# Kernel optimization log

Hardware: AMD Instinct MI355X
Metric: run time of the kernel (lower is better)

The kernel has to match this reference:

```python
import jax, jax.numpy as jnp
import numpy as np

N = 100000   # nodes
E = 600000   # edges
NF = 4       # node feat dim (3 pos + 1 scalar)
EF = 5       # edge feat dim
H = 128      # hidden dim


def setup_inputs() -> dict:
    key = jax.random.key(0)
    ks = jax.random.split(key, 9)

    def lin(k, fan_in, fan_out):
        return (jax.random.normal(k, (fan_in, fan_out), dtype=jnp.float32)
                * (1.0 / np.sqrt(fan_in)))

    x = jax.random.normal(ks[0], (N, NF), dtype=jnp.float32)
    edge_index = jax.random.randint(ks[1], (2, E), 0, N, dtype=jnp.int32)
    edge_attr = jax.random.normal(ks[2], (E, EF), dtype=jnp.float32)

    return {
        "x": x,
        "edge_attr": edge_attr,
        "W1": lin(ks[3], NF, H), "b1": jnp.zeros((H,), jnp.float32),
        "W2": lin(ks[4], H, H),  "b2": jnp.zeros((H,), jnp.float32),
        "Wm1": lin(ks[5], 2 * H + EF, H), "bm1": jnp.zeros((H,), jnp.float32),
        "Wm2": lin(ks[6], H, H),          "bm2": jnp.zeros((H,), jnp.float32),
        "Wm3": lin(ks[7], H, 1),          "bm3": jnp.zeros((1,), jnp.float32),
        "edge_index": edge_index,
    }


def reference(x, edge_attr, W1, b1, W2, b2, Wm1, bm1, Wm2, bm2, Wm3, bm3,
              edge_index):
    src, dst = edge_index[0], edge_index[1]
    n = x.shape[0]

    # GCNConv: add self-loops, symmetric D^{-1/2} A D^{-1/2} normalization.
    loop = jnp.arange(n, dtype=src.dtype)
    src_sl = jnp.concatenate([src, loop])
    dst_sl = jnp.concatenate([dst, loop])
    deg = jax.ops.segment_sum(jnp.ones_like(src_sl, dtype=x.dtype),
                              dst_sl, num_segments=n)
    dinv = jnp.where(deg > 0, jax.lax.rsqrt(deg), 0.0)
    enorm = dinv[src_sl] * dinv[dst_sl]          # [E + N]

    def gcn(h, W, b):
        h = h @ W                                 # transform then propagate
        msg = h[src_sl] * enorm[:, None]          # gather + scale
        return jax.ops.segment_sum(msg, dst_sl, num_segments=n) + b

    h = jax.nn.relu(gcn(x, W1, b1))
    h = gcn(h, W2, b2)

    # Edge classifier: gather endpoints, concat with edge features, MLP.
    edge_emb = jnp.concatenate([h[src], h[dst], edge_attr], axis=1)  # [E, 2H+EF]
    z = jax.nn.relu(edge_emb @ Wm1 + bm1)
    z = jax.nn.relu(z @ Wm2 + bm2)
    out = (z @ Wm3 + bm3)[:, 0]
    return jax.nn.sigmoid(out)
```

## Files before the change

kernel.cpp:

```cpp
#include <hip/hip_runtime.h>
#include <math.h>

#define TPB 256
#define SCAN_T 256
#define SCAN_I 4
#define SCAN_CHUNK 1024

typedef __attribute__((ext_vector_type(8))) short bf16x8;
typedef __attribute__((ext_vector_type(16))) float f32x16;

static __device__ __forceinline__ short f2bf(float a) {
  unsigned ua = __builtin_bit_cast(unsigned, a);
  ua = (ua + 0x7fffu + ((ua >> 16) & 1u)) >> 16;
  return (short)ua;
}
static __device__ __forceinline__ unsigned f2bf_pack(float a, float b) {
  unsigned ua = __builtin_bit_cast(unsigned, a);
  unsigned ub = __builtin_bit_cast(unsigned, b);
  ua = (ua + 0x7fffu + ((ua >> 16) & 1u)) >> 16;
  ub = (ub + 0x7fffu + ((ub >> 16) & 1u)) >> 16;
  return ua | (ub << 16);
}
static __device__ __forceinline__ float bflo(unsigned u) {
  return __builtin_bit_cast(float, u << 16);
}
static __device__ __forceinline__ float bfhi(unsigned u) {
  return __builtin_bit_cast(float, u & 0xffff0000u);
}

__global__ void k_zero_int(int* __restrict__ p, int n) {
  int t = blockIdx.x * TPB + threadIdx.x;
  if (t < n) p[t] = 0;
}

__global__ void k_hist(const int* __restrict__ dst, int* __restrict__ deg, int E) {
  int t = blockIdx.x * TPB + threadIdx.x;
  if (t < E) atomicAdd(&deg[dst[t]], 1);
}

__global__ __launch_bounds__(SCAN_T) void k_scan_local(const int* __restrict__ deg,
                                                       int* __restrict__ loc,
                                                       int* __restrict__ bsum,
                                                       float* __restrict__ dinv,
                                                       const float4* __restrict__ x4,
                                                       float4* __restrict__ xs, int N) {
  __shared__ int s[SCAN_T];
  int b = blockIdx.x, t = threadIdx.x;
  int base = b * SCAN_CHUNK + t * SCAN_I;
  int v[SCAN_I];
  int sum = 0;
#pragma unroll
  for (int u = 0; u < SCAN_I; u++) {
    int x = (base + u < N) ? deg[base + u] : 0;
    if (base + u < N) {
      float dv = rsqrtf((float)x + 1.0f);
      dinv[base + u] = dv;
      float4 xv = x4[base + u];
      xs[base + u] = make_float4(xv.x * dv, xv.y * dv, xv.z * dv, xv.w * dv);
    }
    v[u] = sum;
    sum += x;
  }
  s[t] = sum;
  __syncthreads();
#pragma unroll
  for (int off = 1; off < SCAN_T; off <<= 1) {
    int x = (t >= off) ? s[t - off] : 0;
    __syncthreads();
    s[t] += x;
    __syncthreads();
  }
  int excl = (t == 0) ? 0 : s[t - 1];
#pragma unroll
  for (int u = 0; u < SCAN_I; u++)
    if (base + u < N) loc[base + u] = v[u] + excl;
  if (t == SCAN_T - 1) bsum[b] = s[t];
}

__global__ void k_scan_block(int* __restrict__ bsum, int nb) {
  int t = threadIdx.x;
  int i0 = 2 * t, i1 = 2 * t + 1;
  int a = (i0 < nb) ? bsum[i0] : 0;
  int b = (i1 < nb) ? bsum[i1] : 0;
  int s = a + b;
#pragma unroll
  for (int off = 1; off < 64; off <<= 1) {
    int u = __shfl_up(s, off, 64);
    if (t >= off) s += u;
  }
  int excl = s - (a + b);
  if (i0 < nb) bsum[i0] = excl;
  if (i1 < nb) bsum[i1] = excl + a;
}

__global__ void k_scan_add(int* __restrict__ rowoff, const int* __restrict__ bsum,
                           int* __restrict__ cursor, int N) {
  int t = blockIdx.x * TPB + threadIdx.x;
  if (t >= N) return;
  int ro = rowoff[t] + bsum[t / SCAN_CHUNK];
  rowoff[t] = ro;
  cursor[t] = ro;
}

__global__ void k_fill_slots(const int* __restrict__ src, const int* __restrict__ dst,
                             int* __restrict__ cursor, int* __restrict__ slots,
                             int2* __restrict__ epair, int E) {
  int e = blockIdx.x * TPB + threadIdx.x;
  if (e >= E) return;
  int d = dst[e];
  int pos = atomicAdd(&cursor[d], 1);
  slots[pos] = src[e];
  epair[pos] = make_int2(e, d);
}

__global__ __launch_bounds__(256) void k_agg1(const float4* __restrict__ xs,
                                              const int* __restrict__ rowoff,
                                              const int* __restrict__ deg,
                                              const int* __restrict__ slots,
                                              const float* __restrict__ dinv,
                                              const float* __restrict__ W1,
                                              const float* __restrict__ b1,
                                              unsigned* __restrict__ h1, int N) {
  int u = threadIdx.x & 15;
  float w[4][8];
  float bb[8];
#pragma unroll
  for (int k = 0; k < 4; k++)
#pragma unroll
    for (int c = 0; c < 8; c++) w[k][c] = W1[k * 128 + u * 8 + c];
#pragma unroll
  for (int c = 0; c < 8; c++) bb[c] = b1[u * 8 + c];

  int g0 = (blockIdx.x * TPB + threadIdx.x) >> 4;
  int gstride = (gridDim.x * TPB) >> 4;
  for (int n = g0; n < N; n += gstride) {
    int start = rowoff[n], d = deg[n];
    float4 acc = make_float4(0.f, 0.f, 0.f, 0.f);
    for (int j = u; j < d; j += 16) {
      float4 v = xs[slots[start + j]];
      acc.x += v.x;
      acc.y += v.y;
      acc.z += v.z;
      acc.w += v.w;
    }
#pragma unroll
    for (int off = 8; off >= 1; off >>= 1) {
      acc.x += __shfl_xor(acc.x, off, 16);
      acc.y += __shfl_xor(acc.y, off, 16);
      acc.z += __shfl_xor(acc.z, off, 16);
      acc.w += __shfl_xor(acc.w, off, 16);
    }
    float4 xv = xs[n];
    acc.x += xv.x;
    acc.y += xv.y;
    acc.z += xv.z;
    acc.w += xv.w;
    float sc = dinv[n];
    uint4 o;
    unsigned* op = (unsigned*)&o;
#pragma unroll
    for (int c2 = 0; c2 < 4; c2++) {
      int c0 = 2 * c2, c1 = 2 * c2 + 1;
      float r0 = fmaf(acc.x, w[0][c0],
                      fmaf(acc.y, w[1][c0], fmaf(acc.z, w[2][c0], acc.w * w[3][c0])));
      float r1 = fmaf(acc.x, w[0][c1],
                      fmaf(acc.y, w[1][c1], fmaf(acc.z, w[2][c1], acc.w * w[3][c1])));
      r0 = fmaxf(fmaf(r0, sc, bb[c0]), 0.f);
      r1 = fmaxf(fmaf(r1, sc, bb[c1]), 0.f);
      op[c2] = f2bf_pack(r0, r1);
    }
    *(uint4*)&h1[(size_t)n * 64 + u * 4] = o;
  }
}

template <bool RELU>
__global__ void k_agg(const unsigned* __restrict__ ts, const int* __restrict__ rowoff,
                      const int* __restrict__ deg, const int* __restrict__ slots,
                      const float* __restrict__ dinv, const float* __restrict__ bias,
                      unsigned* __restrict__ hout, int N) {
  int t = blockIdx.x * TPB + threadIdx.x;
  int n = t >> 4;
  if (n >= N) return;
  int q = (t & 15) << 2;
  uint4 sv = *(const uint4*)&ts[(size_t)n * 64 + q];
  float a0 = bflo(sv.x), a1 = bfhi(sv.x), a2 = bflo(sv.y), a3 = bfhi(sv.y);
  float a4 = bflo(sv.z), a5 = bfhi(sv.z), a6 = bflo(sv.w), a7 = bfhi(sv.w);
  int start = rowoff[n], d = deg[n];
  for (int j0 = 0; j0 < d; j0 += 8) {
    int sl[8];
#pragma unroll
    for (int u = 0; u < 8; u++) {
      int jj = j0 + u;
      sl[u] = (jj < d) ? slots[start + jj] : -1;
    }
    uint4 v[8];
#pragma unroll
    for (int u = 0; u < 8; u++)
      v[u] = (sl[u] >= 0) ? *(const uint4*)&ts[(size_t)sl[u] * 64 + q]
                          : make_uint4(0u, 0u, 0u, 0u);
#pragma unroll
    for (int u = 0; u < 8; u++) {
      a0 += bflo(v[u].x);
      a1 += bfhi(v[u].x);
      a2 += bflo(v[u].y);
      a3 += bfhi(v[u].y);
      a4 += bflo(v[u].z);
      a5 += bfhi(v[u].z);
      a6 += bflo(v[u].w);
      a7 += bfhi(v[u].w);
    }
  }
  float sc = dinv[n];
  int col = q << 1;
  float4 b0 = *(const float4*)&bias[col];
  float4 b1 = *(const float4*)&bias[col + 4];
  a0 = a0 * sc + b0.x;
  a1 = a1 * sc + b0.y;
  a2 = a2 * sc + b0.z;
  a3 = a3 * sc + b0.w;
  a4 = a4 * sc + b1.x;
  a5 = a5 * sc + b1.y;
  a6 = a6 * sc + b1.z;
  a7 = a7 * sc + b1.w;
  if (RELU) {
    a0 = fmaxf(a0, 0.f);
    a1 = fmaxf(a1, 0.f);
    a2 = fmaxf(a2, 0.f);
    a3 = fmaxf(a3, 0.f);
    a4 = fmaxf(a4, 0.f);
    a5 = fmaxf(a5, 0.f);
    a6 = fmaxf(a6, 0.f);
    a7 = fmaxf(a7, 0.f);
  }
  uint4 p;
  p.x = f2bf_pack(a0, a1);
  p.y = f2bf_pack(a2, a3);
  p.z = f2bf_pack(a4, a5);
  p.w = f2bf_pack(a6, a7);
  *(uint4*)&hout[(size_t)n * 64 + q] = p;
}

template <bool BIAS, bool DINV>
__global__ __launch_bounds__(256, 2) void k_gemm_bf(const unsigned* __restrict__ A,
                                                    const float* __restrict__ W,
                                                    const float* __restrict__ bias,
                                                    const float* __restrict__ dinv,
                                                    unsigned* __restrict__ out, int N) {
  __shared__ unsigned sA[64 * 64];
  __shared__ float sDinv[64];
  int tid = threadIdx.x;
  int wv = tid >> 6, lane = tid & 63;
  int rg = wv >> 1, ch = wv & 1;
  int l31 = lane & 31, h = lane >> 5;

  bf16x8 wf[2][8];
  float bcol[2];
#pragma unroll
  for (int t = 0; t < 2; t++) {
    int col = ch * 64 + 2 * l31 + t;
#pragma unroll
    for (int kk = 0; kk < 8; kk++) {
      int kb = kk * 16 + h * 8;
      bf16x8 v;
#pragma unroll
      for (int u = 0; u < 8; u++) v[u] = f2bf(W[(kb + u) * 128 + col]);
      wf[t][kk] = v;
    }
    bcol[t] = BIAS ? bias[col] : 0.f;
  }

  int ntiles = (N + 63) >> 6;
  for (int tile = blockIdx.x; tile < ntiles; tile += gridDim.x) {
    __syncthreads();
    int row0 = tile << 6;
    for (int idx = tid; idx < 1024; idx += 256) {
      int r = idx >> 4, c4 = idx & 15;
      int n = row0 + r;
      uint4 v = (n < N) ? ((const uint4*)A)[(size_t)n * 16 + c4] : make_uint4(0, 0, 0, 0);
      *(uint4*)&sA[r * 64 + ((c4 * 4) ^ ((r & 15) << 2))] = v;
    }
    if (DINV && tid < 64) sDinv[tid] = (row0 + tid < N) ? dinv[row0 + tid] : 0.f;
    __syncthreads();

    int arow = rg * 32 + l31;
    const char* abase = (const char*)sA + arow * 256;
    int swz = (arow & 15) << 4;
    f32x16 acc[2];
#pragma unroll
    for (int t = 0; t < 2; t++) {
#pragma unroll
      for (int r = 0; r < 16; r++) acc[t][r] = 0.f;
    }
#pragma unroll
    for (int kk = 0; kk < 8; kk++) {
      bf16x8 a = *(const bf16x8*)(abase + ((kk * 32 + h * 16) ^ swz));
      acc[0] = __builtin_amdgcn_mfma_f32_32x32x16_bf16(a, wf[0][kk], acc[0], 0, 0, 0);
      acc[1] = __builtin_amdgcn_mfma_f32_32x32x16_bf16(a, wf[1][kk], acc[1], 0, 0, 0);
    }
#pragma unroll
    for (int r = 0; r < 16; r++) {
      int drow = (r & 3) + 8 * (r >> 2) + 4 * h;
      int n = row0 + rg * 32 + drow;
      if (n < N) {
        float v0 = acc[0][r] + bcol[0];
        float v1 = acc[1][r] + bcol[1];
        if (DINV) {
          float s = sDinv[rg * 32 + drow];
          v0 *= s;
          v1 *= s;
        }
        out[(size_t)n * 64 + ch * 32 + l31] = f2bf_pack(v0, v1);
      }
    }
  }
}

__global__ __launch_bounds__(512, 2) void k_gemm_dual(const unsigned* __restrict__ A,
                                                      const float* __restrict__ Wm1,
                                                      const float* __restrict__ bm1,
                                                      unsigned* __restrict__ out_s,
                                                      unsigned* __restrict__ out_d, int N) {
  __shared__ unsigned sA[64 * 64];
  int tid = threadIdx.x;
  int wv = tid >> 6, lane = tid & 63;
  int part = wv >> 2;
  int w4 = wv & 3;
  int rg = w4 >> 1, ch = w4 & 1;
  int l31 = lane & 31, h = lane >> 5;
  const float* W = Wm1 + (size_t)part * 128 * 128;
  unsigned* outp = part ? out_d : out_s;

  bf16x8 wf[2][8];
  float bcol[2];
#pragma unroll
  for (int t = 0; t < 2; t++) {
    int col = ch * 64 + 2 * l31 + t;
#pragma unroll
    for (int kk = 0; kk < 8; kk++) {
      int kb = kk * 16 + h * 8;
      bf16x8 v;
#pragma unroll
      for (int u = 0; u < 8; u++) v[u] = f2bf(W[(kb + u) * 128 + col]);
      wf[t][kk] = v;
    }
    bcol[t] = part ? 0.f : bm1[col];
  }

  int ntiles = (N + 63) >> 6;
  for (int tile = blockIdx.x; tile < ntiles; tile += gridDim.x) {
    __syncthreads();
    int row0 = tile << 6;
    for (int idx = tid; idx < 1024; idx += 512) {
      int r = idx >> 4, c4 = idx & 15;
      int n = row0 + r;
      uint4 v = (n < N) ? ((const uint4*)A)[(size_t)n * 16 + c4] : make_uint4(0, 0, 0, 0);
      *(uint4*)&sA[r * 64 + ((c4 * 4) ^ ((r & 15) << 2))] = v;
    }
    __syncthreads();

    int arow = rg * 32 + l31;
    const char* abase = (const char*)sA + arow * 256;
    int swz = (arow & 15) << 4;
    f32x16 acc[2];
#pragma unroll
    for (int t = 0; t < 2; t++) {
#pragma unroll
      for (int r = 0; r < 16; r++) acc[t][r] = 0.f;
    }
#pragma unroll
    for (int kk = 0; kk < 8; kk++) {
      bf16x8 a = *(const bf16x8*)(abase + ((kk * 32 + h * 16) ^ swz));
      acc[0] = __builtin_amdgcn_mfma_f32_32x32x16_bf16(a, wf[0][kk], acc[0], 0, 0, 0);
      acc[1] = __builtin_amdgcn_mfma_f32_32x32x16_bf16(a, wf[1][kk], acc[1], 0, 0, 0);
    }
#pragma unroll
    for (int r = 0; r < 16; r++) {
      int drow = (r & 3) + 8 * (r >> 2) + 4 * h;
      int n = row0 + rg * 32 + drow;
      if (n < N) {
        float v0 = acc[0][r] + bcol[0];
        float v1 = acc[1][r] + bcol[1];
        outp[(size_t)n * 64 + ch * 32 + l31] = f2bf_pack(v0, v1);
      }
    }
  }
}

__global__ __launch_bounds__(256, 3) void k_edge_mlp(
    const unsigned* __restrict__ a_s, const unsigned* __restrict__ a_d,
    const float* __restrict__ eattr, const int* __restrict__ slots,
    const int2* __restrict__ epair, const float* __restrict__ We,
    const float* __restrict__ Wm2, const float* __restrict__ bm2,
    const float* __restrict__ Wm3, const float* __restrict__ bm3,
    float* __restrict__ out, int E) {
  __shared__ unsigned sZ1[64 * 64];
  __shared__ float sEa[64][5];
  __shared__ int sSrc[64], sDst[64], sEid[64];
  __shared__ float sP[64][2];

  int tid = threadIdx.x;
  int wv = tid >> 6;
  int lane = tid & 63;
  int rg = wv >> 1;
  int ch = wv & 1;
  int l31 = lane & 31;
  int h = lane >> 5;

  bf16x8 bfr[2][8];
#pragma unroll
  for (int t = 0; t < 2; t++) {
    int col = ch * 64 + t * 32 + l31;
#pragma unroll
    for (int kk = 0; kk < 8; kk++) {
      int kb = kk * 16 + h * 8;
      bf16x8 v;
#pragma unroll
      for (int u = 0; u < 8; u++) v[u] = f2bf(Wm2[(kb + u) * 128 + col]);
      bfr[t][kk] = v;
    }
  }
  float wm3c[2], bm2c[2];
#pragma unroll
  for (int t = 0; t < 2; t++) {
    int col = ch * 64 + t * 32 + l31;
    wm3c[t] = Wm3[col];
    bm2c[t] = bm2[col];
  }
  float bm3v = bm3[0];
  float2 we[5];
#pragma unroll
  for (int j = 0; j < 5; j++) we[j] = *(const float2*)(We + j * 128 + 2 * lane);

  int ntiles = (E + 63) >> 6;
  for (int tile = blockIdx.x; tile < ntiles; tile += gridDim.x) {
    __syncthreads();
    int p0 = tile << 6;
    if (tid < 64) {
      int p = p0 + tid;
      int2 ed = (p < E) ? epair[p] : make_int2(0, 0);
      sSrc[tid] = (p < E) ? slots[p] : 0;
      sDst[tid] = ed.y;
      sEid[tid] = ed.x;
    }
    for (int idx = tid; idx < 320; idx += 256) {
      int r = idx / 5, j = idx - r * 5;
      int p = p0 + r;
      int e = (p < E) ? epair[p].x : 0;
      sEa[r][j] = (p < E) ? eattr[(size_t)e * 5 + j] : 0.f;
    }
    __syncthreads();

    unsigned ua[16], ud[16];
#pragma unroll
    for (int i = 0; i < 16; i++) {
      int r = wv * 16 + i;
      ua[i] = a_s[(size_t)sSrc[r] * 64 + lane];
      ud[i] = a_d[(size_t)sDst[r] * 64 + lane];
    }
#pragma unroll
    for (int i = 0; i < 16; i++) {
      int r = wv * 16 + i;
      float v0 = bflo(ua[i]) + bflo(ud[i]);
      float v1 = bfhi(ua[i]) + bfhi(ud[i]);
#pragma unroll
      for (int j = 0; j < 5; j++) {
        float ea = sEa[r][j];
        v0 = fmaf(ea, we[j].x, v0);
        v1 = fmaf(ea, we[j].y, v1);
      }
      v0 = fmaxf(v0, 0.f);
      v1 = fmaxf(v1, 0.f);
      sZ1[r * 64 + (lane ^ ((r & 15) << 2))] = f2bf_pack(v0, v1);
    }
    __syncthreads();

    int arow = rg * 32 + l31;
    const char* abase = (const char*)sZ1 + arow * 256;
    int swz = (arow & 15) << 4;
    float p16[16];
#pragma unroll
    for (int r = 0; r < 16; r++) p16[r] = 0.f;
#pragma unroll
    for (int t = 0; t < 2; t++) {
      f32x16 acc;
#pragma unroll
      for (int r = 0; r < 16; r++) acc[r] = 0.f;
#pragma unroll
      for (int kk = 0; kk < 8; kk++) {
        bf16x8 a = *(const bf16x8*)(abase + ((kk * 32 + h * 16) ^ swz));
        acc = __builtin_amdgcn_mfma_f32_32x32x16_bf16(a, bfr[t][kk], acc, 0, 0, 0);
      }
#pragma unroll
      for (int r = 0; r < 16; r++) {
        float z2 = fmaxf(acc[r] + bm2c[t], 0.f);
        p16[r] = fmaf(z2, wm3c[t], p16[r]);
      }
    }
#pragma unroll
    for (int r = 0; r < 16; r++) {
      float p = p16[r];
#pragma unroll
      for (int off = 16; off >= 1; off >>= 1) p += __shfl_xor(p, off, 32);
      if (l31 == 0) {
        int row = (r & 3) + 8 * (r >> 2) + 4 * h;
        sP[rg * 32 + row][ch] = p;
      }
    }
    __syncthreads();
    if (tid < 64) {
      int p = p0 + tid;
      if (p < E) {
        float pv = sP[tid][0] + sP[tid][1] + bm3v;
        out[sEid[tid]] = 1.f / (1.f + __expf(-pv));
      }
    }
  }
}

extern "C" void kernel_launch(void* const* d_in, const int* in_sizes, int n_in,
                              void* d_out, int out_size, void* d_ws, size_t ws_size,
                              hipStream_t stream) {
  const float* x = (const float*)d_in[0];
  const float* eattr = (const float*)d_in[1];
  const float* W1 = (const float*)d_in[2];
  const float* b1 = (const float*)d_in[3];
  const float* W2 = (const float*)d_in[4];
  const float* b2 = (const float*)d_in[5];
  const float* Wm1 = (const float*)d_in[6];
  const float* bm1 = (const float*)d_in[7];
  const float* Wm2 = (const float*)d_in[8];
  const float* bm2 = (const float*)d_in[9];
  const float* Wm3 = (const float*)d_in[10];
  const float* bm3 = (const float*)d_in[11];
  const int* ei = (const int*)d_in[12];
  int N = in_sizes[0] / 4;
  int E = in_sizes[12] / 2;
  const int* src = ei;
  const int* dst = ei + E;
  float* out = (float*)d_out;

  size_t npad = (size_t)((N + 63) & ~63);
  float* dinv = (float*)d_ws;
  float4* xs = (float4*)(dinv + npad);
  unsigned* U1 = (unsigned*)(xs + npad);
  unsigned* U2 = U1 + (size_t)N * 64;
  unsigned* U3 = U2 + (size_t)N * 64;
  unsigned* U4 = U3 + (size_t)N * 64;
  int* degi = (int*)(U4 + (size_t)N * 64);
  int* rowoff = degi + npad;
  int* cursor = rowoff + npad;
  int* bsum = cursor + npad;
  int* slots = bsum + 256;
  int2* epair = (int2*)(slots + ((E + 1) & ~1));

  int gN = (N + TPB - 1) / TPB;
  int gE = (E + TPB - 1) / TPB;
  int gN16 = (N * 16 + TPB - 1) / TPB;
  int nb1 = (N + SCAN_CHUNK - 1) / SCAN_CHUNK;

  k_zero_int<<<gN, TPB, 0, stream>>>(degi, N);
  k_hist<<<gE, TPB, 0, stream>>>(dst, degi, E);
  k_scan_local<<<nb1, SCAN_T, 0, stream>>>(degi, rowoff, bsum, dinv, (const float4*)x, xs, N);
  k_scan_block<<<1, 64, 0, stream>>>(bsum, nb1);
  k_scan_add<<<gN, TPB, 0, stream>>>(rowoff, bsum, cursor, N);
  k_fill_slots<<<gE, TPB, 0, stream>>>(src, dst, cursor, slots, epair, E);

  k_agg1<<<2048, TPB, 0, stream>>>(xs, rowoff, degi, slots, dinv, W1, b1, U2, N);

  k_gemm_bf<false, true><<<512, TPB, 0, stream>>>(U2, W2, nullptr, dinv, U1, N);
  k_agg<false><<<gN16, TPB, 0, stream>>>(U1, rowoff, degi, slots, dinv, b2, U3, N);

  k_gemm_dual<<<512, 512, 0, stream>>>(U3, Wm1, bm1, U2, U4, N);
  k_edge_mlp<<<2048, TPB, 0, stream>>>(U2, U4, eattr, slots, epair,
                                       Wm1 + 256 * 128, Wm2, bm2, Wm3, bm3, out, E);
}
```

Baseline: 281.6 us.

## Double-buffer edge metadata and prefetch next tile's source rows during MFMA

Software-pipelines the persistent edge-MLP loop. The next tile's indices and edge attributes are staged into a second shared buffer, and the next tile's a_s gathers are issued into registers before the MFMA stage of the current tile. The aim is to hide gather latency behind compute. In exchange it adds register pressure from keeping 16 prefetched values live across the MFMA, plus an extra barrier per tile.

```diff
diff --git a/kernel.cpp b/kernel.cpp
--- a/kernel.cpp
+++ b/kernel.cpp
@@ -394,8 +394,8 @@
     const float* __restrict__ Wm3, const float* __restrict__ bm3,
     float* __restrict__ out, int E) {
   __shared__ unsigned sZ1[64 * 64];
-  __shared__ float sEa[64][5];
-  __shared__ int sSrc[64], sDst[64], sEid[64];
+  __shared__ float sEa[2][64][5];
+  __shared__ int sSrc[2][64], sDst[2][64], sEid[2][64];
   __shared__ float sP[64][2];
 
   int tid = threadIdx.x;
@@ -432,31 +432,45 @@
   for (int j = 0; j < 5; j++) we[j] = *(const float2*)(We + j * 128 + 2 * lane);
 
   int ntiles = (E + 63) >> 6;
-  for (int tile = blockIdx.x; tile < ntiles; tile += gridDim.x) {
-    __syncthreads();
-    int p0 = tile << 6;
+
+  auto stage = [&](int t, int b) {
+    bool tv = t < ntiles;
     if (tid < 64) {
-      int p = p0 + tid;
-      int2 ed = (p < E) ? epair[p] : make_int2(0, 0);
-      sSrc[tid] = (p < E) ? slots[p] : 0;
-      sDst[tid] = ed.y;
-      sEid[tid] = ed.x;
+      int p = (t << 6) + tid;
+      bool v = tv && (p < E);
+      int2 ed = v ? epair[p] : make_int2(0, 0);
+      sSrc[b][tid] = v ? slots[p] : 0;
+      sDst[b][tid] = ed.y;
+      sEid[b][tid] = ed.x;
     }
     for (int idx = tid; idx < 320; idx += 256) {
       int r = idx / 5, j = idx - r * 5;
-      int p = p0 + r;
-      int e = (p < E) ? epair[p].x : 0;
-      sEa[r][j] = (p < E) ? eattr[(size_t)e * 5 + j] : 0.f;
-    }
-    __syncthreads();
-
-    unsigned ua[16], ud[16];
-#pragma unroll
-    for (int i = 0; i < 16; i++) {
-      int r = wv * 16 + i;
-      ua[i] = a_s[(size_t)sSrc[r] * 64 + lane];
-      ud[i] = a_d[(size_t)sDst[r] * 64 + lane];
-    }
+      int p = (t << 6) + r;
+      bool v = tv && (p < E);
+      int e = v ? epair[p].x : 0;
+      sEa[b][r][j] = v ? eattr[(size_t)e * 5 + j] : 0.f;
+    }
+  };
+
+  int tile0 = blockIdx.x;
+  if (tile0 >= ntiles) return;
+
+  stage(tile0, 0);
+  __syncthreads();
+  unsigned ua[16];
+#pragma unroll
+  for (int i = 0; i < 16; i++)
+    ua[i] = a_s[(size_t)sSrc[0][wv * 16 + i] * 64 + lane];
+
+  int c = 0;
+  for (int tile = tile0; tile < ntiles; tile += gridDim.x, c ^= 1) {
+    stage(tile + gridDim.x, c ^ 1);
+
+    unsigned ud[16];
+#pragma unroll
+    for (int i = 0; i < 16; i++)
+      ud[i] = a_d[(size_t)sDst[c][wv * 16 + i] * 64 + lane];
+
 #pragma unroll
     for (int i = 0; i < 16; i++) {
       int r = wv * 16 + i;
@@ -464,7 +478,7 @@
       float v1 = bfhi(ua[i]) + bfhi(ud[i]);
 #pragma unroll
       for (int j = 0; j < 5; j++) {
-        float ea = sEa[r][j];
+        float ea = sEa[c][r][j];
         v0 = fmaf(ea, we[j].x, v0);
         v1 = fmaf(ea, we[j].y, v1);
       }
@@ -473,6 +487,12 @@
       sZ1[r * 64 + (lane ^ ((r & 15) << 2))] = f2bf_pack(v0, v1);
     }
     __syncthreads();
+
+    if (tile + gridDim.x < ntiles) {
+#pragma unroll
+      for (int i = 0; i < 16; i++)
+        ua[i] = a_s[(size_t)sSrc[c ^ 1][wv * 16 + i] * 64 + lane];
+    }
 
     int arow = rg * 32 + l31;
     const char* abase = (const char*)sZ1 + arow * 256;
@@ -507,13 +527,15 @@
       }
     }
     __syncthreads();
+
     if (tid < 64) {
-      int p = p0 + tid;
+      int p = (tile << 6) + tid;
       if (p < E) {
         float pv = sP[tid][0] + sP[tid][1] + bm3v;
-        out[sEid[tid]] = 1.f / (1.f + __expf(-pv));
-      }
-    }
+        out[sEid[c][tid]] = 1.f / (1.f + __expf(-pv));
+      }
+    }
+    __syncthreads();
   }
 }
 
```

Measured after the change: 412.4 us. 1.46x slower.
